# Kernel optimization log

Measured on AMD Instinct MI355X. Metric: run time of the kernel, lower is better.

## Reference

```python
import jax, jax.numpy as jnp
import numpy as np

N_VARS = 32
D_MODEL = 256
D_MECH = 128
D_NOISE = D_MODEL // 4
N_LAYERS = 3
TEMP = 0.5
BATCH = 512


def gelu(x):
    return jax.nn.gelu(x, approximate=False)  # torch nn.GELU default is exact erf


def setup_inputs() -> dict:
    key = jax.random.key(0)
    ks = jax.random.split(key, 12)
    n, d, m, dn = N_VARS, D_MODEL, D_MECH, D_NOISE
    return {
        "exogenous_noise": jax.random.normal(ks[0], (BATCH, n, dn), dtype=jnp.float32),
        # learned params (edge_logits init randn*0.5 for a nontrivial adjacency)
        "edge_logits": jax.random.normal(ks[1], (n, n), dtype=jnp.float32) * 0.5,
        "var_emb": jax.random.normal(ks[2], (n, d), dtype=jnp.float32) * 0.02,
        # shared parent_aggregate Linear(d, d); weights stored [in, out]
        "pa_W": jax.random.normal(ks[3], (d, d), dtype=jnp.float32) / np.sqrt(d).astype(np.float32),
        "pa_b": jnp.zeros((d,), dtype=jnp.float32),
        # per-variable mechanism MLP weights, stacked on variable axis
        "m_W1": jax.random.normal(ks[4], (n, d, m), dtype=jnp.float32) / np.sqrt(d).astype(np.float32),
        "m_b1": jnp.zeros((n, m), dtype=jnp.float32),
        "m_W2": jax.random.normal(ks[5], (n, m, m), dtype=jnp.float32) / np.sqrt(m).astype(np.float32),
        "m_b2": jnp.zeros((n, m), dtype=jnp.float32),
        "m_W3": jax.random.normal(ks[6], (n, m, d), dtype=jnp.float32) / np.sqrt(m).astype(np.float32),
        "m_b3": jnp.zeros((n, d), dtype=jnp.float32),
        # per-variable noise encoder Linear(dn, d)
        "ne_W": jax.random.normal(ks[7], (n, dn, d), dtype=jnp.float32) / np.sqrt(dn).astype(np.float32),
        "ne_b": jnp.zeros((n, d), dtype=jnp.float32),
    }


def _forward(exogenous_noise, edge_logits, var_emb, pa_W, pa_b,
             m_W1, m_b1, m_W2, m_b2, m_W3, m_b3, ne_W, ne_b):
    n, d = N_VARS, D_MODEL
    batch = exogenous_noise.shape[0]
    # eval-mode adjacency: sigmoid(masked_logits / temp); diagonal masked out
    diag_mask = 1.0 - jnp.eye(n, dtype=edge_logits.dtype)
    adj = jax.nn.sigmoid((edge_logits * diag_mask) / jnp.asarray(TEMP, edge_logits.dtype))
    adj_cols = adj.T                                  # row i = adj[:, i], parents of var i
    noise_t = jnp.transpose(exogenous_noise, (1, 0, 2))  # (n, batch, dn)

    values0 = jnp.zeros((batch, n, d), dtype=exogenous_noise.dtype)
    idx = jnp.arange(n)
    xs = (idx, adj_cols, var_emb, noise_t, m_W1, m_b1, m_W2, m_b2, m_W3, m_b3, ne_W, ne_b)

    def var_step(values, x):
        i, a_col, emb_i, nz, w1, b1, w2, b2, w3, b3, nw, nb = x
        # adjacency-weighted aggregation over ALL current values (sequentially updated)
        pc = jnp.einsum('v,bvd->bd', a_col, values)
        parent_input = gelu((pc + emb_i) @ pa_W + pa_b)
        h = gelu(parent_input @ w1 + b1)
        h = gelu(h @ w2 + b2)
        out = h @ w3 + b3
        out = out + gelu(nz @ nw + nb)               # noise encoder contribution
        values = values.at[:, i].set(out)
        return values, None

    values = values0
    for _ in range(N_LAYERS):
        values, _ = jax.lax.scan(var_step, values, xs)
    return values


def reference(exogenous_noise, edge_logits, var_emb, pa_W, pa_b,
              m_W1, m_b1, m_W2, m_b2, m_W3, m_b3, ne_W, ne_b):
    return _forward(exogenous_noise, edge_logits, var_emb, pa_W, pa_b,
                    m_W1, m_b1, m_W2, m_b2, m_W3, m_b3, ne_W, ne_b)
```

## Files before the change

kernel.cpp:

```cpp
#include <hip/hip_runtime.h>


typedef __bf16 bf16x8 __attribute__((ext_vector_type(8)));
typedef float  f32x4  __attribute__((ext_vector_type(4)));

#define N_VARS 32
#define BTILE 4
#define NBLK 128

#define WS_ADJB   0
#define WS_B3P    4096
#define WS_EMBP   36864
#define WS_WSB    69632
#define ELOFF_PA  0
#define ELOFF_W1  65536
#define ELOFF_W2  1114112
#define ELOFF_W3  1638400
#define ELOFF_W3P 2686976
#define WS_H2B    7540736

#define XSTR 272
#define HSTR 144
#define VSTR 40

__device__ __forceinline__ unsigned short f2b(float f) {
    unsigned u = __float_as_uint(f);
    u += 0x7FFFu + ((u >> 16) & 1u);
    return (unsigned short)(u >> 16);
}

__device__ __forceinline__ float b2f(unsigned short u) {
    return __uint_as_float(((unsigned)u) << 16);
}

__device__ __forceinline__ void bar_lds() {
    asm volatile("s_waitcnt lgkmcnt(0)\n\ts_barrier" ::: "memory");
}

__device__ __forceinline__ float gelu_e(float x) {
    float z  = x * 0.7071067811865476f;
    float az = fabsf(z);
    float t  = __builtin_amdgcn_rcpf(1.0f + 0.47047f * az);
    float p  = t * (0.3480242f + t * (-0.0958798f + t * 0.7478556f));
    float e  = 1.0f - p * __expf(-z * z);
    float er = (z < 0.0f) ? -e : e;
    return 0.5f * x * (1.0f + er);
}

__device__ __forceinline__ float pickq(f32x4 v, int q) {
    float lo = (q & 1) ? v[1] : v[0];
    float hi = (q & 1) ? v[3] : v[2];
    return (q & 2) ? hi : lo;
}

#define MFMA16(a, b, c) __builtin_amdgcn_mfma_f32_16x16x32_bf16(a, b, c, 0, 0, 0)

__global__ void prep_all(const float* __restrict__ paW, const float* __restrict__ mW1,
                         const float* __restrict__ mW2, const float* __restrict__ mW3,
                         const float* __restrict__ edge, unsigned short* __restrict__ wsb,
                         unsigned short* __restrict__ adjb,
                         const float* __restrict__ noise, const float* __restrict__ neW,
                         const float* __restrict__ neb, float* __restrict__ outp,
                         const float* __restrict__ mb3, const float* __restrict__ emb,
                         const float* __restrict__ pab,
                         float* __restrict__ b3P, float* __restrict__ embP) {
    __shared__ unsigned short tile[32 * 256];
    const int c = blockIdx.x, tid = threadIdx.x;
    if (c < 520) {
        const float* src; unsigned short* dst; int N, KS, ks;
        if (c < 8)        { src = paW;                     dst = wsb + ELOFF_PA;             N = 256; KS = 8; ks = c; }
        else if (c < 264) { int v = (c - 8) >> 3;   ks = (c - 8) & 7;
                            src = mW1 + v * 32768;         dst = wsb + ELOFF_W1 + v * 32768; N = 128; KS = 8; }
        else if (c < 392) { int v = (c - 264) >> 2; ks = (c - 264) & 3;
                            src = mW2 + v * 16384;         dst = wsb + ELOFF_W2 + v * 16384; N = 128; KS = 4; }
        else              { int v = (c - 392) >> 2; ks = (c - 392) & 3;
                            src = mW3 + v * 32768;         dst = wsb + ELOFF_W3 + v * 32768; N = 256; KS = 4; }
        const int kb = ks * 32, nsh = (N == 256) ? 8 : 7;
        for (int t = tid; t < 32 * N; t += 256) {
            int r = t >> nsh, col = t & (N - 1);
            tile[r * N + col] = f2b(src[(kb + r) * N + col]);
        }
        __syncthreads();
        const int nout = (N >> 4) * 64;
        for (int o = tid; o < nout; o += 256) {
            int nt = o >> 6, lane = o & 63;
            int n = nt * 16 + (lane & 15), k0 = (lane >> 4) << 3;
            unsigned e[8];
            #pragma unroll
            for (int j = 0; j < 8; j++) e[j] = tile[(k0 + j) * N + n];
            uint4 pk;
            pk.x = e[0] | (e[1] << 16); pk.y = e[2] | (e[3] << 16);
            pk.z = e[4] | (e[5] << 16); pk.w = e[6] | (e[7] << 16);
            *(uint4*)(dst + ((nt * KS + ks) * 64 + lane) * 8) = pk;
        }
    } else if (c == 520) {
        for (int t = tid; t < 1024; t += 256) {
            int v = t >> 5, ci = t & 31;
            float x = edge[t];
            float m = (v == ci) ? 0.0f : x;
            float a = __builtin_amdgcn_rcpf(1.0f + __expf(-2.0f * m));
            unsigned short hi = f2b(a);
            float rem = a - b2f(hi);
            adjb[ci * 64 + v]      = hi;
            adjb[ci * 64 + 32 + v] = f2b(rem);
        }
    } else if (c < 1545) {
        int sb = c - 521;
        int i = sb >> 5, g = sb & 31, d = tid;
        float w[64];
        #pragma unroll
        for (int k = 0; k < 64; k++) w[k] = neW[(i * 64 + k) * 256 + d];
        float bias = neb[i * 256 + d];
        for (int bb = 0; bb < 16; bb++) {
            int b = g * 16 + bb;
            const float* nr = noise + (b * 32 + i) * 64;
            float a0 = bias, a1 = 0.f, a2 = 0.f, a3 = 0.f;
            #pragma unroll
            for (int k = 0; k < 16; k++) {
                a0 += nr[4 * k + 0] * w[4 * k + 0];
                a1 += nr[4 * k + 1] * w[4 * k + 1];
                a2 += nr[4 * k + 2] * w[4 * k + 2];
                a3 += nr[4 * k + 3] * w[4 * k + 3];
            }
            outp[(b * 32 + i) * 256 + d] = gelu_e((a0 + a1) + (a2 + a3));
        }
    } else if (c < 2057) {
        const int idx = c - 1545;
        const int v = idx >> 4, mg = (idx & 15) * 8;
        const int d = tid;
        const float* w3r = mW3 + (size_t)(v * 128 + mg) * 256;
        float acc[8];
        #pragma unroll
        for (int r = 0; r < 8; r++) acc[r] = 0.f;
        for (int n = 0; n < 256; n++) {
            float pa = paW[n * 256 + d];
            #pragma unroll
            for (int r = 0; r < 8; r++) acc[r] += w3r[r * 256 + n] * pa;
        }
        const int ks = mg >> 5, lg = (mg >> 3) & 3;
        const int nt = d >> 4, lane = lg * 16 + (d & 15);
        uint4 pk;
        pk.x = (unsigned)f2b(acc[0]) | ((unsigned)f2b(acc[1]) << 16);
        pk.y = (unsigned)f2b(acc[2]) | ((unsigned)f2b(acc[3]) << 16);
        pk.z = (unsigned)f2b(acc[4]) | ((unsigned)f2b(acc[5]) << 16);
        pk.w = (unsigned)f2b(acc[6]) | ((unsigned)f2b(acc[7]) << 16);
        *(uint4*)(wsb + ELOFF_W3P + v * 32768 + ((nt * 4 + ks) * 64 + lane) * 8) = pk;
    } else if (c < 2089) {
        const int v = c - 2057;
        float a = 0.f;
        for (int n = 0; n < 256; n++) a += mb3[v * 256 + n] * paW[n * 256 + tid];
        b3P[v * 256 + tid] = a;
    } else {
        const int v = c - 2089;
        float a = pab[tid];
        for (int n = 0; n < 256; n++) a += emb[v * 256 + n] * paW[n * 256 + tid];
        embP[v * 256 + tid] = a;
    }
}

__global__ __launch_bounds__(512, 2) void
scm_main(const float* __restrict__ embP, const float* __restrict__ b3Pp,
         const float* __restrict__ mb1, const float* __restrict__ mb2,
         const unsigned short* __restrict__ adjb,
         const __bf16* __restrict__ wsbf, const float* __restrict__ outp,
         unsigned short* __restrict__ h2buf) {
    __shared__ unsigned short valsP[1024 * VSTR];
    __shared__ unsigned short ne2S[4 * 32 * 256];
    __shared__ unsigned short X2[4 * XSTR];
    __shared__ unsigned short Hs1[4 * HSTR];
    __shared__ unsigned short Hs2[4 * HSTR];

    const int tid = threadIdx.x, blk = blockIdx.x;

    {
        uint4 z; z.x = z.y = z.z = z.w = 0;
        for (int k = tid; k < 5120; k += 512) ((uint4*)valsP)[k] = z;
    }

    const int wid = tid >> 6, lane = tid & 63, l15 = lane & 15, q = lane >> 4;
    const int l3 = l15 & 3;
    const int nW = wid * 16 + l15;
    const int n0 = nW, n1 = nW + 128;

    {
        const int R = wid * 16 + l15;
        const float* src = outp + ((size_t)(blk * BTILE + (R >> 5)) * 32 + (R & 31)) * 256 + q * 8;
        bf16x8 afr[8];
        #pragma unroll
        for (int ks = 0; ks < 8; ks++) {
            float4 x0 = *(const float4*)(src + ks * 32);
            float4 x1 = *(const float4*)(src + ks * 32 + 4);
            uint4 pk;
            pk.x = (unsigned)f2b(x0.x) | ((unsigned)f2b(x0.y) << 16);
            pk.y = (unsigned)f2b(x0.z) | ((unsigned)f2b(x0.w) << 16);
            pk.z = (unsigned)f2b(x1.x) | ((unsigned)f2b(x1.y) << 16);
            pk.w = (unsigned)f2b(x1.z) | ((unsigned)f2b(x1.w) << 16);
            afr[ks] = __builtin_bit_cast(bf16x8, pk);
        }
        #pragma unroll 4
        for (int nt = 0; nt < 16; nt++) {
            f32x4 e4 = {0, 0, 0, 0}, o4 = {0, 0, 0, 0};
            #pragma unroll
            for (int ks = 0; ks < 8; ks += 2) {
                bf16x8 b0 = *(const bf16x8*)(wsbf + ELOFF_PA + ((nt * 8 + ks) * 64 + lane) * 8);
                bf16x8 b1 = *(const bf16x8*)(wsbf + ELOFF_PA + ((nt * 8 + ks + 1) * 64 + lane) * 8);
                e4 = MFMA16(afr[ks], b0, e4);
                o4 = MFMA16(afr[ks + 1], b1, o4);
            }
            f32x4 a = e4 + o4;
            #pragma unroll
            for (int rr = 0; rr < 4; rr++) {
                int R2 = wid * 16 + q * 4 + rr;
                ne2S[R2 * 256 + nt * 16 + l15] = f2b(a[rr]);
            }
        }
    }

    X2[q * XSTR + n0] = f2b(gelu_e(embP[n0]));
    X2[q * XSTR + n1] = f2b(gelu_e(embP[n1]));
    bar_lds();

    auto step = [&](int s, bf16x8 (&w1f)[8], bf16x8 (&w1n)[8]) {
        const int i = s & 31, ni = (s + 1) & 31;
        const bool last = s >= 64;

        #pragma unroll
        for (int ks = 0; ks < 8; ks++)
            w1n[ks] = *(const bf16x8*)(wsbf + ELOFF_W1 + (size_t)ni * 32768 +
                                       ((wid * 8 + ks) * 64 + lane) * 8);
        bf16x8 w2f[4], wPf0[4], wPf1[4];
        #pragma unroll
        for (int ks = 0; ks < 4; ks++) {
            w2f[ks]  = *(const bf16x8*)(wsbf + ELOFF_W2 + (size_t)i * 16384 +
                                        ((wid * 4 + ks) * 64 + lane) * 8);
            wPf0[ks] = *(const bf16x8*)(wsbf + ELOFF_W3P + (size_t)i * 32768 +
                                        ((wid * 4 + ks) * 64 + lane) * 8);
            wPf1[ks] = *(const bf16x8*)(wsbf + ELOFF_W3P + (size_t)i * 32768 +
                                        (((wid + 8) * 4 + ks) * 64 + lane) * 8);
        }
        float bi1 = mb1[i * 128 + nW];
        float bi2 = mb2[i * 128 + nW];
        const float ne2_0 = b2f(ne2S[(q * 32 + i) * 256 + n0]);
        const float ne2_1 = b2f(ne2S[(q * 32 + i) * 256 + n1]);
        const float b3P0 = b3Pp[i * 256 + n0];
        const float b3P1 = b3Pp[i * 256 + n1];
        const float eP0 = embP[ni * 256 + n0];
        const float eP1 = embP[ni * 256 + n1];
        bf16x8 anh = *(const bf16x8*)(adjb + ni * 64 + q * 8);
        bf16x8 anl = *(const bf16x8*)(adjb + ni * 64 + 32 + q * 8);
        const float ani = b2f(adjb[ni * 64 + i]) + b2f(adjb[ni * 64 + 32 + i]);

        {
            f32x4 aa = {0, 0, 0, 0}, ab = {0, 0, 0, 0};
            f32x4 ac = {0, 0, 0, 0}, ad = {0, 0, 0, 0};
            #pragma unroll
            for (int ks = 0; ks < 8; ks += 4) {
                bf16x8 af0 = *(const bf16x8*)(X2 + l3 * XSTR + ks * 32 + q * 8);
                bf16x8 af1 = *(const bf16x8*)(X2 + l3 * XSTR + (ks + 1) * 32 + q * 8);
                bf16x8 af2 = *(const bf16x8*)(X2 + l3 * XSTR + (ks + 2) * 32 + q * 8);
                bf16x8 af3 = *(const bf16x8*)(X2 + l3 * XSTR + (ks + 3) * 32 + q * 8);
                aa = MFMA16(af0, w1f[ks], aa);
                ab = MFMA16(af1, w1f[ks + 1], ab);
                ac = MFMA16(af2, w1f[ks + 2], ac);
                ad = MFMA16(af3, w1f[ks + 3], ad);
            }
            float sb = (pickq(aa, q) + pickq(ab, q)) +
                       (pickq(ac, q) + pickq(ad, q)) + bi1;
            Hs1[q * HSTR + nW] = f2b(gelu_e(sb));
        }
        bar_lds();

        float pc0 = 0.f, pc1 = 0.f, oP0, oP1;
        {
            f32x4 ca = {0, 0, 0, 0}, cb = {0, 0, 0, 0};
            #pragma unroll
            for (int ks = 0; ks < 4; ks += 2) {
                bf16x8 af0 = *(const bf16x8*)(Hs1 + l3 * HSTR + ks * 32 + q * 8);
                bf16x8 af1 = *(const bf16x8*)(Hs1 + l3 * HSTR + (ks + 1) * 32 + q * 8);
                ca = MFMA16(af0, w2f[ks], ca);
                cb = MFMA16(af1, w2f[ks + 1], cb);
            }
            #pragma unroll
            for (int t = 0; t < 4; t++) {
                bf16x8 vf0 = *(const bf16x8*)(valsP + (t * 256 + n0) * VSTR + q * 8);
                bf16x8 vf1 = *(const bf16x8*)(valsP + (t * 256 + n1) * VSTR + q * 8);
                f32x4 z = {0, 0, 0, 0};
                f32x4 p0 = MFMA16(anl, vf0, MFMA16(anh, vf0, z));
                f32x4 p1 = MFMA16(anl, vf1, MFMA16(anh, vf1, z));
                pc0 = (q == t) ? p0[0] : pc0;
                pc1 = (q == t) ? p1[0] : pc1;
            }
            oP0 = b2f(valsP[(q * 256 + n0) * VSTR + i]);
            oP1 = b2f(valsP[(q * 256 + n1) * VSTR + i]);
            float scv = pickq(ca, q) + pickq(cb, q) + bi2;
            unsigned short hv = f2b(gelu_e(scv));
            Hs2[q * HSTR + nW] = hv;
            if (last)
                h2buf[((size_t)i * 512 + blk * BTILE + q) * 128 + nW] = hv;
        }
        bar_lds();

        {
            f32x4 c0a = {0, 0, 0, 0}, c0b = {0, 0, 0, 0};
            f32x4 c1a = {0, 0, 0, 0}, c1b = {0, 0, 0, 0};
            #pragma unroll
            for (int ks = 0; ks < 4; ks += 2) {
                bf16x8 af0 = *(const bf16x8*)(Hs2 + l3 * HSTR + ks * 32 + q * 8);
                bf16x8 af1 = *(const bf16x8*)(Hs2 + l3 * HSTR + (ks + 1) * 32 + q * 8);
                c0a = MFMA16(af0, wPf0[ks], c0a);
                c1a = MFMA16(af0, wPf1[ks], c1a);
                c0b = MFMA16(af1, wPf0[ks + 1], c0b);
                c1b = MFMA16(af1, wPf1[ks + 1], c1b);
            }
            float nP0 = pickq(c0a, q) + pickq(c0b, q) + b3P0 + ne2_0;
            float nP1 = pickq(c1a, q) + pickq(c1b, q) + b3P1 + ne2_1;
            unsigned short ur0 = f2b(nP0), ur1 = f2b(nP1);
            valsP[(q * 256 + n0) * VSTR + i] = ur0;
            valsP[(q * 256 + n1) * VSTR + i] = ur1;
            float x0 = pc0 + ani * (b2f(ur0) - oP0) + eP0;
            float x1 = pc1 + ani * (b2f(ur1) - oP1) + eP1;
            X2[q * XSTR + n0] = f2b(gelu_e(x0));
            X2[q * XSTR + n1] = f2b(gelu_e(x1));
        }
        bar_lds();
    };

    bf16x8 w1a[8], w1b[8];
    #pragma unroll
    for (int ks = 0; ks < 8; ks++)
        w1a[ks] = *(const bf16x8*)(wsbf + ELOFF_W1 +
                                   ((wid * 8 + ks) * 64 + lane) * 8);
    for (int ss = 0; ss < 48; ss++) {
        step(2 * ss,     w1a, w1b);
        step(2 * ss + 1, w1b, w1a);
    }
}

__global__ __launch_bounds__(256) void
post_out(const unsigned short* __restrict__ h2buf, const __bf16* __restrict__ wsbf,
         const float* __restrict__ mb3, float* __restrict__ outp) {
    const int tid = threadIdx.x;
    const int wid = tid >> 6, lane = tid & 63, l15 = lane & 15, q = lane >> 4;
    const int gid = blockIdx.x * 4 + wid;
    const int i = gid >> 5, bt = gid & 31;
    bf16x8 af[4];
    #pragma unroll
    for (int ks = 0; ks < 4; ks++)
        af[ks] = *(const bf16x8*)(h2buf + ((size_t)i * 512 + bt * 16 + l15) * 128 +
                                  ks * 32 + q * 8);
    #pragma unroll 4
    for (int nt = 0; nt < 16; nt++) {
        f32x4 e4 = {0, 0, 0, 0}, o4 = {0, 0, 0, 0};
        #pragma unroll
        for (int ks = 0; ks < 4; ks += 2) {
            bf16x8 b0 = *(const bf16x8*)(wsbf + ELOFF_W3 + (size_t)i * 32768 +
                                         ((nt * 4 + ks) * 64 + lane) * 8);
            bf16x8 b1 = *(const bf16x8*)(wsbf + ELOFF_W3 + (size_t)i * 32768 +
                                         ((nt * 4 + ks + 1) * 64 + lane) * 8);
            e4 = MFMA16(af[ks], b0, e4);
            o4 = MFMA16(af[ks + 1], b1, o4);
        }
        f32x4 a = e4 + o4;
        float bv = mb3[i * 256 + nt * 16 + l15];
        #pragma unroll
        for (int rr = 0; rr < 4; rr++) {
            int b = bt * 16 + q * 4 + rr;
            size_t o = ((size_t)b * 32 + i) * 256 + nt * 16 + l15;
            outp[o] = a[rr] + bv + outp[o];
        }
    }
}

extern "C" void kernel_launch(void* const* d_in, const int* in_sizes, int n_in,
                              void* d_out, int out_size, void* d_ws, size_t ws_size,
                              hipStream_t stream) {
    (void)in_sizes; (void)n_in; (void)out_size; (void)ws_size;
    const float* noise = (const float*)d_in[0];
    const float* edge  = (const float*)d_in[1];
    const float* emb   = (const float*)d_in[2];
    const float* paW   = (const float*)d_in[3];
    const float* pab   = (const float*)d_in[4];
    const float* mW1   = (const float*)d_in[5];
    const float* mb1   = (const float*)d_in[6];
    const float* mW2   = (const float*)d_in[7];
    const float* mb2   = (const float*)d_in[8];
    const float* mW3   = (const float*)d_in[9];
    const float* mb3   = (const float*)d_in[10];
    const float* neW   = (const float*)d_in[11];
    const float* neb   = (const float*)d_in[12];
    float* outp = (float*)d_out;

    unsigned short* adjb = (unsigned short*)((char*)d_ws + WS_ADJB);
    float* b3P  = (float*)((char*)d_ws + WS_B3P);
    float* embP = (float*)((char*)d_ws + WS_EMBP);
    unsigned short* wsb  = (unsigned short*)((char*)d_ws + WS_WSB);
    unsigned short* h2b  = (unsigned short*)((char*)d_ws + WS_H2B);

    prep_all<<<2121, 256, 0, stream>>>(paW, mW1, mW2, mW3, edge, wsb, adjb,
                                       noise, neW, neb, outp, mb3, emb, pab,
                                       b3P, embP);
    scm_main<<<NBLK, 512, 0, stream>>>(embP, b3P, mb1, mb2, adjb,
                                       (const __bf16*)wsb, outp, h2b);
    post_out<<<256, 256, 0, stream>>>(h2b, (const __bf16*)wsb, mb3, outp);
}
```

Measured before the change: 396.7 us.

## Software-pipeline all per-step weight loads one step ahead with explicit vmcnt

Every global load a step needs (W1, W2, W3P fragments, biases, and the next step's embP) is now issued one step ahead into a double-buffered register set through inline asm loads, with an explicit s_waitcnt so the wait covers only the previous set. The adjacency matrix is copied into LDS once, and b3P is folded into ne2S at setup, which removes per-step global reads. The aim is to hide global-memory latency on the serial 96-step chain. In exchange, register pressure rises under a 512-thread, 2-blocks-per-SM bound. The hand-written vmcnt accounting is fragile if the compiler emits other memory ops, such as the h2buf stores.

```diff
diff --git a/kernel.cpp b/kernel.cpp
--- a/kernel.cpp
+++ b/kernel.cpp
@@ -54,6 +54,11 @@
 }
 
 #define MFMA16(a, b, c) __builtin_amdgcn_mfma_f32_16x16x32_bf16(a, b, c, 0, 0, 0)
+
+#define GLD4(dst, ptr) asm volatile("global_load_dwordx4 %0, %1, off" \
+                                    : "=v"(dst) : "v"(ptr))
+#define GLD1(dst, ptr) asm volatile("global_load_dword %0, %1, off" \
+                                    : "=v"(dst) : "v"(ptr))
 
 __global__ void prep_all(const float* __restrict__ paW, const float* __restrict__ mW1,
                          const float* __restrict__ mW2, const float* __restrict__ mW3,
@@ -166,6 +171,7 @@
          unsigned short* __restrict__ h2buf) {
     __shared__ unsigned short valsP[1024 * VSTR];
     __shared__ unsigned short ne2S[4 * 32 * 256];
+    __shared__ unsigned short adjS[2048];
     __shared__ unsigned short X2[4 * XSTR];
     __shared__ unsigned short Hs1[4 * HSTR];
     __shared__ unsigned short Hs2[4 * HSTR];
@@ -175,6 +181,8 @@
     {
         uint4 z; z.x = z.y = z.z = z.w = 0;
         for (int k = tid; k < 5120; k += 512) ((uint4*)valsP)[k] = z;
+        for (int k = tid; k < 1024; k += 512)
+            ((unsigned*)adjS)[k] = ((const unsigned*)adjb)[k];
     }
 
     const int wid = tid >> 6, lane = tid & 63, l15 = lane & 15, q = lane >> 4;
@@ -211,7 +219,8 @@
             #pragma unroll
             for (int rr = 0; rr < 4; rr++) {
                 int R2 = wid * 16 + q * 4 + rr;
-                ne2S[R2 * 256 + nt * 16 + l15] = f2b(a[rr]);
+                ne2S[R2 * 256 + nt * 16 + l15] =
+                    f2b(a[rr] + b3Pp[(R2 & 31) * 256 + nt * 16 + l15]);
             }
         }
     }
@@ -220,35 +229,47 @@
     X2[q * XSTR + n1] = f2b(gelu_e(embP[n1]));
     bar_lds();
 
-    auto step = [&](int s, bf16x8 (&w1f)[8], bf16x8 (&w1n)[8]) {
+    struct WSet {
+        uint4 w1[8]; uint4 w2[4]; uint4 p0[4]; uint4 p1[4];
+        float s0, s1, s2, s3;
+    };
+
+    auto issue_set = [&](WSet& S, int st) {
+        const int it = st & 31, nt2 = (st + 1) & 31;
+        const __bf16* b1 = wsbf + ELOFF_W1 + (size_t)it * 32768 +
+                           ((size_t)(wid * 8) * 64 + lane) * 8;
+        #pragma unroll
+        for (int ks = 0; ks < 8; ks++) GLD4(S.w1[ks], b1 + ks * 512);
+        const __bf16* b2 = wsbf + ELOFF_W2 + (size_t)it * 16384 +
+                           ((size_t)(wid * 4) * 64 + lane) * 8;
+        #pragma unroll
+        for (int ks = 0; ks < 4; ks++) GLD4(S.w2[ks], b2 + ks * 512);
+        const __bf16* bp = wsbf + ELOFF_W3P + (size_t)it * 32768 +
+                           ((size_t)(wid * 4) * 64 + lane) * 8;
+        #pragma unroll
+        for (int ks = 0; ks < 4; ks++) GLD4(S.p0[ks], bp + ks * 512);
+        const __bf16* bq = bp + 16384;
+        #pragma unroll
+        for (int ks = 0; ks < 4; ks++) GLD4(S.p1[ks], bq + ks * 512);
+        GLD1(S.s0, mb1 + it * 128 + nW);
+        GLD1(S.s1, mb2 + it * 128 + nW);
+        GLD1(S.s2, embP + nt2 * 256 + n0);
+        GLD1(S.s3, embP + nt2 * 256 + n1);
+    };
+
+    auto step = [&](int s, const WSet& cur, WSet& nxt) {
         const int i = s & 31, ni = (s + 1) & 31;
         const bool last = s >= 64;
 
-        #pragma unroll
-        for (int ks = 0; ks < 8; ks++)
-            w1n[ks] = *(const bf16x8*)(wsbf + ELOFF_W1 + (size_t)ni * 32768 +
-                                       ((wid * 8 + ks) * 64 + lane) * 8);
-        bf16x8 w2f[4], wPf0[4], wPf1[4];
-        #pragma unroll
-        for (int ks = 0; ks < 4; ks++) {
-            w2f[ks]  = *(const bf16x8*)(wsbf + ELOFF_W2 + (size_t)i * 16384 +
-                                        ((wid * 4 + ks) * 64 + lane) * 8);
-            wPf0[ks] = *(const bf16x8*)(wsbf + ELOFF_W3P + (size_t)i * 32768 +
-                                        ((wid * 4 + ks) * 64 + lane) * 8);
-            wPf1[ks] = *(const bf16x8*)(wsbf + ELOFF_W3P + (size_t)i * 32768 +
-                                        (((wid + 8) * 4 + ks) * 64 + lane) * 8);
-        }
-        float bi1 = mb1[i * 128 + nW];
-        float bi2 = mb2[i * 128 + nW];
+        issue_set(nxt, s + 1);
+        asm volatile("s_waitcnt vmcnt(24)");
+        __builtin_amdgcn_sched_barrier(0);
+
         const float ne2_0 = b2f(ne2S[(q * 32 + i) * 256 + n0]);
         const float ne2_1 = b2f(ne2S[(q * 32 + i) * 256 + n1]);
-        const float b3P0 = b3Pp[i * 256 + n0];
-        const float b3P1 = b3Pp[i * 256 + n1];
-        const float eP0 = embP[ni * 256 + n0];
-        const float eP1 = embP[ni * 256 + n1];
-        bf16x8 anh = *(const bf16x8*)(adjb + ni * 64 + q * 8);
-        bf16x8 anl = *(const bf16x8*)(adjb + ni * 64 + 32 + q * 8);
-        const float ani = b2f(adjb[ni * 64 + i]) + b2f(adjb[ni * 64 + 32 + i]);
+        bf16x8 anh = *(const bf16x8*)(adjS + ni * 64 + q * 8);
+        bf16x8 anl = *(const bf16x8*)(adjS + ni * 64 + 32 + q * 8);
+        const float ani = b2f(adjS[ni * 64 + i]) + b2f(adjS[ni * 64 + 32 + i]);
 
         {
             f32x4 aa = {0, 0, 0, 0}, ab = {0, 0, 0, 0};
@@ -259,13 +280,13 @@
                 bf16x8 af1 = *(const bf16x8*)(X2 + l3 * XSTR + (ks + 1) * 32 + q * 8);
                 bf16x8 af2 = *(const bf16x8*)(X2 + l3 * XSTR + (ks + 2) * 32 + q * 8);
                 bf16x8 af3 = *(const bf16x8*)(X2 + l3 * XSTR + (ks + 3) * 32 + q * 8);
-                aa = MFMA16(af0, w1f[ks], aa);
-                ab = MFMA16(af1, w1f[ks + 1], ab);
-                ac = MFMA16(af2, w1f[ks + 2], ac);
-                ad = MFMA16(af3, w1f[ks + 3], ad);
+                aa = MFMA16(af0, __builtin_bit_cast(bf16x8, cur.w1[ks]), aa);
+                ab = MFMA16(af1, __builtin_bit_cast(bf16x8, cur.w1[ks + 1]), ab);
+                ac = MFMA16(af2, __builtin_bit_cast(bf16x8, cur.w1[ks + 2]), ac);
+                ad = MFMA16(af3, __builtin_bit_cast(bf16x8, cur.w1[ks + 3]), ad);
             }
             float sb = (pickq(aa, q) + pickq(ab, q)) +
-                       (pickq(ac, q) + pickq(ad, q)) + bi1;
+                       (pickq(ac, q) + pickq(ad, q)) + cur.s0;
             Hs1[q * HSTR + nW] = f2b(gelu_e(sb));
         }
         bar_lds();
@@ -277,8 +298,8 @@
             for (int ks = 0; ks < 4; ks += 2) {
                 bf16x8 af0 = *(const bf16x8*)(Hs1 + l3 * HSTR + ks * 32 + q * 8);
                 bf16x8 af1 = *(const bf16x8*)(Hs1 + l3 * HSTR + (ks + 1) * 32 + q * 8);
-                ca = MFMA16(af0, w2f[ks], ca);
-                cb = MFMA16(af1, w2f[ks + 1], cb);
+                ca = MFMA16(af0, __builtin_bit_cast(bf16x8, cur.w2[ks]), ca);
+                cb = MFMA16(af1, __builtin_bit_cast(bf16x8, cur.w2[ks + 1]), cb);
             }
             #pragma unroll
             for (int t = 0; t < 4; t++) {
@@ -292,7 +313,7 @@
             }
             oP0 = b2f(valsP[(q * 256 + n0) * VSTR + i]);
             oP1 = b2f(valsP[(q * 256 + n1) * VSTR + i]);
-            float scv = pickq(ca, q) + pickq(cb, q) + bi2;
+            float scv = pickq(ca, q) + pickq(cb, q) + cur.s1;
             unsigned short hv = f2b(gelu_e(scv));
             Hs2[q * HSTR + nW] = hv;
             if (last)
@@ -307,32 +328,31 @@
             for (int ks = 0; ks < 4; ks += 2) {
                 bf16x8 af0 = *(const bf16x8*)(Hs2 + l3 * HSTR + ks * 32 + q * 8);
                 bf16x8 af1 = *(const bf16x8*)(Hs2 + l3 * HSTR + (ks + 1) * 32 + q * 8);
-                c0a = MFMA16(af0, wPf0[ks], c0a);
-                c1a = MFMA16(af0, wPf1[ks], c1a);
-                c0b = MFMA16(af1, wPf0[ks + 1], c0b);
-                c1b = MFMA16(af1, wPf1[ks + 1], c1b);
-            }
-            float nP0 = pickq(c0a, q) + pickq(c0b, q) + b3P0 + ne2_0;
-            float nP1 = pickq(c1a, q) + pickq(c1b, q) + b3P1 + ne2_1;
+                c0a = MFMA16(af0, __builtin_bit_cast(bf16x8, cur.p0[ks]), c0a);
+                c1a = MFMA16(af0, __builtin_bit_cast(bf16x8, cur.p1[ks]), c1a);
+                c0b = MFMA16(af1, __builtin_bit_cast(bf16x8, cur.p0[ks + 1]), c0b);
+                c1b = MFMA16(af1, __builtin_bit_cast(bf16x8, cur.p1[ks + 1]), c1b);
+            }
+            float nP0 = pickq(c0a, q) + pickq(c0b, q) + ne2_0;
+            float nP1 = pickq(c1a, q) + pickq(c1b, q) + ne2_1;
             unsigned short ur0 = f2b(nP0), ur1 = f2b(nP1);
             valsP[(q * 256 + n0) * VSTR + i] = ur0;
             valsP[(q * 256 + n1) * VSTR + i] = ur1;
-            float x0 = pc0 + ani * (b2f(ur0) - oP0) + eP0;
-            float x1 = pc1 + ani * (b2f(ur1) - oP1) + eP1;
+            float x0 = pc0 + ani * (b2f(ur0) - oP0) + cur.s2;
+            float x1 = pc1 + ani * (b2f(ur1) - oP1) + cur.s3;
             X2[q * XSTR + n0] = f2b(gelu_e(x0));
             X2[q * XSTR + n1] = f2b(gelu_e(x1));
         }
         bar_lds();
     };
 
-    bf16x8 w1a[8], w1b[8];
-    #pragma unroll
-    for (int ks = 0; ks < 8; ks++)
-        w1a[ks] = *(const bf16x8*)(wsbf + ELOFF_W1 +
-                                   ((wid * 8 + ks) * 64 + lane) * 8);
+    WSet A, B;
+    issue_set(A, 0);
+    asm volatile("s_waitcnt vmcnt(0)");
+    __builtin_amdgcn_sched_barrier(0);
     for (int ss = 0; ss < 48; ss++) {
-        step(2 * ss,     w1a, w1b);
-        step(2 * ss + 1, w1b, w1a);
+        step(2 * ss,     A, B);
+        step(2 * ss + 1, B, A);
     }
 }
 
```

After: 386.4 us. 2.6% less time.
